# Performance work log

Measured on AMD Instinct MI355X. Metric: run time of the kernel, lower is better.

Reference implementation:

```python
import jax, jax.numpy as jnp
import numpy as np

MASK_VALUE = -1e10  # matches module's -10000000000.0


def setup_inputs() -> dict:
    key = jax.random.key(0)
    k1, k2, k3, k4, k5 = jax.random.split(key, 5)
    B, NQ, NKV, D = 32, 32, 8, 128
    NUM_PAGES, TPP, PAGES_PER_SLOT = 4096, 16, 128
    query = jax.random.normal(k1, (B, 1, NQ, D), dtype=jnp.float32)
    key_pages = jax.random.normal(k2, (NKV, NUM_PAGES, TPP, D), dtype=jnp.float32)
    value_pages = jax.random.normal(k3, (NKV, NUM_PAGES, TPP, D), dtype=jnp.float32)
    page_map = jax.random.randint(k4, (B, PAGES_PER_SLOT), 0, NUM_PAGES, dtype=jnp.int32)
    seq_lengths = jax.random.randint(k5, (B,), 1, PAGES_PER_SLOT * TPP + 1, dtype=jnp.int32)
    return {
        "query": query,
        "key_pages": key_pages,
        "value_pages": value_pages,
        "page_map": page_map,
        "seq_lengths": seq_lengths,
    }


def reference(query, key_pages, value_pages, page_map, seq_lengths):
    """Paged attention, decode mode (single query token per sequence, GQA).

    query:       [B, 1, NQ, D]
    key_pages:   [NKV, NUM_PAGES, TPP, D]
    value_pages: [NKV, NUM_PAGES, TPP, D]
    page_map:    [B, P] page indices per sequence
    seq_lengths: [B] valid kv tokens per sequence
    """
    B, _, NQ, D = query.shape
    NKV, _, TPP, _ = key_pages.shape
    G = NQ // NKV  # GQA group size
    # take last query position -> [B, NKV, G, D]
    q = query[:, -1].reshape(B, NKV, G, D)
    # gather pages per sequence: [NKV, B, P, TPP, D] -> [B, NKV, S, D]
    k = jnp.moveaxis(key_pages[:, page_map], 0, 1).reshape(B, NKV, -1, D)
    v = jnp.moveaxis(value_pages[:, page_map], 0, 1).reshape(B, NKV, -1, D)
    S = k.shape[2]
    scores = jnp.einsum("bkgd,bksd->bkgs", q, k)  # [B, NKV, G, S]
    valid = jnp.arange(S)[None, :] < seq_lengths[:, None]  # [B, S]
    scores = jnp.where(valid[:, None, None, :], scores, MASK_VALUE)
    weights = jax.nn.softmax(scores, axis=-1)
    out = jnp.einsum("bkgs,bksd->bkgd", weights, v)  # [B, NKV, G, D]
    return out.reshape(B, 1, NQ, D)
```

## Files before the change

kernel.cpp:

```cpp
#include <hip/hip_runtime.h>
#include <math.h>

#define NB      32
#define NKV     8
#define NQ      32
#define GQ      4
#define DH      128
#define TPP     16
#define PPS     128
#define NPAGES  4096
#define NSPLIT  8
#define PAGE_F  (TPP*DH)
#define PART_F  (GQ*DH + 2*GQ)

__global__ __launch_bounds__(256) void pa_partial(
    const float* __restrict__ query,
    const float* __restrict__ key_pages,
    const float* __restrict__ value_pages,
    const int*   __restrict__ page_map,
    const int*   __restrict__ seq_lengths,
    float*       __restrict__ ws)
{
    const int blk = blockIdx.x;
    const int sp  = blk & (NSPLIT - 1);
    const int kv  = (blk >> 3) & (NKV - 1);
    const int b   = blk >> 6;
    const int tid = threadIdx.x;

    const int seq     = seq_lengths[b];
    const int n_pages = (seq + TPP - 1) / TPP;
    if (sp >= n_pages) return;

    __shared__ __align__(16) float kbuf[TPP * DH];
    __shared__ __align__(16) float vbuf[TPP * DH];
    __shared__ float s_sc[GQ][TPP];

    const int lane = tid & 63;
    const int wv   = tid >> 6;
    const int tok  = wv * 4 + (lane >> 4);
    const int l16  = lane & 15;
    const int d0   = l16 * 8;

    const int d  = tid & 127;
    const int gA = tid >> 7;
    const int gB = gA + 2;

    float qreg[GQ][8];
    #pragma unroll
    for (int g = 0; g < GQ; ++g) {
        const float4* qp = (const float4*)(query + (size_t)((b * NQ + kv * GQ + g) * DH + d0));
        const float4 a = qp[0], c = qp[1];
        qreg[g][0] = a.x; qreg[g][1] = a.y; qreg[g][2] = a.z; qreg[g][3] = a.w;
        qreg[g][4] = c.x; qreg[g][5] = c.y; qreg[g][6] = c.z; qreg[g][7] = c.w;
    }

    float mA = -INFINITY, mB = -INFINITY;
    float lA = 0.f, lB = 0.f;
    float accA = 0.f, accB = 0.f;

    for (int p = sp; p < n_pages; p += NSPLIT) {
        const int pg = page_map[b * PPS + p];
        const float4* kg = (const float4*)(key_pages   + (size_t)(kv * NPAGES + pg) * PAGE_F);
        const float4* vg = (const float4*)(value_pages + (size_t)(kv * NPAGES + pg) * PAGE_F);

        __syncthreads();
        {
            float4* kb = (float4*)kbuf;
            float4* vb = (float4*)vbuf;
            kb[tid]       = kg[tid];
            kb[tid + 256] = kg[tid + 256];
            vb[tid]       = vg[tid];
            vb[tid + 256] = vg[tid + 256];
        }
        __syncthreads();

        float part0, part1, part2, part3;
        {
            const float4 k0 = *(const float4*)&kbuf[tok * DH + d0];
            const float4 k1 = *(const float4*)&kbuf[tok * DH + d0 + 4];
            part0 = qreg[0][0]*k0.x + qreg[0][1]*k0.y + qreg[0][2]*k0.z + qreg[0][3]*k0.w
                  + qreg[0][4]*k1.x + qreg[0][5]*k1.y + qreg[0][6]*k1.z + qreg[0][7]*k1.w;
            part1 = qreg[1][0]*k0.x + qreg[1][1]*k0.y + qreg[1][2]*k0.z + qreg[1][3]*k0.w
                  + qreg[1][4]*k1.x + qreg[1][5]*k1.y + qreg[1][6]*k1.z + qreg[1][7]*k1.w;
            part2 = qreg[2][0]*k0.x + qreg[2][1]*k0.y + qreg[2][2]*k0.z + qreg[2][3]*k0.w
                  + qreg[2][4]*k1.x + qreg[2][5]*k1.y + qreg[2][6]*k1.z + qreg[2][7]*k1.w;
            part3 = qreg[3][0]*k0.x + qreg[3][1]*k0.y + qreg[3][2]*k0.z + qreg[3][3]*k0.w
                  + qreg[3][4]*k1.x + qreg[3][5]*k1.y + qreg[3][6]*k1.z + qreg[3][7]*k1.w;
            #pragma unroll
            for (int off = 8; off >= 1; off >>= 1) {
                part0 += __shfl_xor(part0, off);
                part1 += __shfl_xor(part1, off);
                part2 += __shfl_xor(part2, off);
                part3 += __shfl_xor(part3, off);
            }
        }
        const int tglob = p * TPP + tok;
        if (l16 < GQ) {
            const float val = (l16 == 0) ? part0 : (l16 == 1) ? part1
                            : (l16 == 2) ? part2 : part3;
            s_sc[l16][tok] = (tglob < seq) ? val : -1e30f;
        }
        __syncthreads();

        float sA[TPP], sB[TPP];
        #pragma unroll
        for (int t = 0; t < TPP; ++t) { sA[t] = s_sc[gA][t]; sB[t] = s_sc[gB][t]; }

        float pA = -1e30f, pB = -1e30f;
        #pragma unroll
        for (int t = 0; t < TPP; ++t) { pA = fmaxf(pA, sA[t]); pB = fmaxf(pB, sB[t]); }

        const float mnA = fmaxf(mA, pA), mnB = fmaxf(mB, pB);
        const float scA = __expf(mA - mnA), scB = __expf(mB - mnB);
        mA = mnA; mB = mnB;

        float sumA = 0.f, sumB = 0.f;
        #pragma unroll
        for (int t = 0; t < TPP; ++t) {
            sA[t] = __expf(sA[t] - mnA); sumA += sA[t];
            sB[t] = __expf(sB[t] - mnB); sumB += sB[t];
        }
        lA = lA * scA + sumA;
        lB = lB * scB + sumB;
        accA *= scA;
        accB *= scB;

        #pragma unroll
        for (int t = 0; t < TPP; ++t) {
            const float v = vbuf[t * DH + d];
            accA += sA[t] * v;
            accB += sB[t] * v;
        }
    }

    float* base = ws + (size_t)blk * PART_F;
    base[gA * DH + d] = accA;
    base[gB * DH + d] = accB;
    if (d == 0) {
        base[GQ * DH + gA]      = mA;
        base[GQ * DH + GQ + gA] = lA;
        base[GQ * DH + gB]      = mB;
        base[GQ * DH + GQ + gB] = lB;
    }
}

__global__ __launch_bounds__(256) void pa_combine(
    const float* __restrict__ ws,
    const int*   __restrict__ seq_lengths,
    float*       __restrict__ out)
{
    const int blk = blockIdx.x;
    const int b   = blk >> 3;
    const int kv  = blk & 7;
    const int tid = threadIdx.x;
    const int d   = tid & 127;
    const int gA  = tid >> 7;
    const int gB  = gA + 2;

    const int seq     = seq_lengths[b];
    const int n_pages = (seq + TPP - 1) / TPP;
    const int ns      = (n_pages < NSPLIT) ? n_pages : NSPLIT;

    const float* base0 = ws + (size_t)blk * NSPLIT * PART_F;

    float MA = -INFINITY, MB = -INFINITY;
    for (int si = 0; si < ns; ++si) {
        const float* p = base0 + si * PART_F;
        MA = fmaxf(MA, p[GQ * DH + gA]);
        MB = fmaxf(MB, p[GQ * DH + gB]);
    }

    float LA = 0.f, LB = 0.f, oA = 0.f, oB = 0.f;
    for (int si = 0; si < ns; ++si) {
        const float* p = base0 + si * PART_F;
        const float eA = __expf(p[GQ * DH + gA] - MA);
        const float eB = __expf(p[GQ * DH + gB] - MB);
        LA += p[GQ * DH + GQ + gA] * eA;
        LB += p[GQ * DH + GQ + gB] * eB;
        oA += p[gA * DH + d] * eA;
        oB += p[gB * DH + d] * eB;
    }

    float* ob = out + (size_t)(b * NQ + kv * GQ) * DH;
    ob[gA * DH + d] = oA / LA;
    ob[gB * DH + d] = oB / LB;
}

extern "C" void kernel_launch(void* const* d_in, const int* in_sizes, int n_in,
                              void* d_out, int out_size, void* d_ws, size_t ws_size,
                              hipStream_t stream)
{
    const float* query       = (const float*)d_in[0];
    const float* key_pages   = (const float*)d_in[1];
    const float* value_pages = (const float*)d_in[2];
    const int*   page_map    = (const int*)d_in[3];
    const int*   seq_lengths = (const int*)d_in[4];
    float*       out         = (float*)d_out;
    float*       ws          = (float*)d_ws;

    pa_partial<<<NB * NKV * NSPLIT, 256, 0, stream>>>(
        query, key_pages, value_pages, page_map, seq_lengths, ws);
    pa_combine<<<NB * NKV, 256, 0, stream>>>(ws, seq_lengths, out);
}
```

Baseline: 61.24 us.

## Double-buffer KV pages in LDS using async global-to-LDS loads

```diff
diff --git a/kernel.cpp b/kernel.cpp
--- a/kernel.cpp
+++ b/kernel.cpp
@@ -1,5 +1,6 @@
 #include <hip/hip_runtime.h>
 #include <math.h>
+#include <stdint.h>
 
 #define NB      32
 #define NKV     8
@@ -12,6 +13,10 @@
 #define NSPLIT  8
 #define PAGE_F  (TPP*DH)
 #define PART_F  (GQ*DH + 2*GQ)
+
+#define GLOAD16(gsrc, ldst) \
+    __builtin_amdgcn_global_load_lds((const __attribute__((address_space(1))) uint32_t*)(gsrc), \
+                                     (__attribute__((address_space(3))) uint32_t*)(ldst), 16, 0, 0)
 
 __global__ __launch_bounds__(256) void pa_partial(
     const float* __restrict__ query,
@@ -31,8 +36,8 @@
     const int n_pages = (seq + TPP - 1) / TPP;
     if (sp >= n_pages) return;
 
-    __shared__ __align__(16) float kbuf[TPP * DH];
-    __shared__ __align__(16) float vbuf[TPP * DH];
+    __shared__ __align__(16) float kbuf[2][TPP * DH];
+    __shared__ __align__(16) float vbuf[2][TPP * DH];
     __shared__ float s_sc[GQ][TPP];
 
     const int lane = tid & 63;
@@ -54,30 +59,36 @@
         qreg[g][4] = c.x; qreg[g][5] = c.y; qreg[g][6] = c.z; qreg[g][7] = c.w;
     }
 
+    const float4* kbase = (const float4*)(key_pages   + (size_t)kv * NPAGES * PAGE_F);
+    const float4* vbase = (const float4*)(value_pages + (size_t)kv * NPAGES * PAGE_F);
+
+    auto stage = [&](int buf, int pg) {
+        const float4* kg = kbase + (size_t)pg * (PAGE_F / 4);
+        const float4* vg = vbase + (size_t)pg * (PAGE_F / 4);
+        GLOAD16(kg + wv * 128 +       lane, &kbuf[buf][wv * 512]);
+        GLOAD16(kg + wv * 128 +  64 + lane, &kbuf[buf][wv * 512 + 256]);
+        GLOAD16(vg + wv * 128 +       lane, &vbuf[buf][wv * 512]);
+        GLOAD16(vg + wv * 128 +  64 + lane, &vbuf[buf][wv * 512 + 256]);
+    };
+
     float mA = -INFINITY, mB = -INFINITY;
     float lA = 0.f, lB = 0.f;
     float accA = 0.f, accB = 0.f;
 
-    for (int p = sp; p < n_pages; p += NSPLIT) {
-        const int pg = page_map[b * PPS + p];
-        const float4* kg = (const float4*)(key_pages   + (size_t)(kv * NPAGES + pg) * PAGE_F);
-        const float4* vg = (const float4*)(value_pages + (size_t)(kv * NPAGES + pg) * PAGE_F);
-
-        __syncthreads();
-        {
-            float4* kb = (float4*)kbuf;
-            float4* vb = (float4*)vbuf;
-            kb[tid]       = kg[tid];
-            kb[tid + 256] = kg[tid + 256];
-            vb[tid]       = vg[tid];
-            vb[tid + 256] = vg[tid + 256];
-        }
-        __syncthreads();
+    stage(0, page_map[b * PPS + sp]);
+    asm volatile("s_waitcnt vmcnt(0)" ::: "memory");
+    __builtin_amdgcn_s_barrier();
+    asm volatile("" ::: "memory");
+
+    int cur = 0;
+    for (int p = sp; p < n_pages; p += NSPLIT, cur ^= 1) {
+        const int pn = p + NSPLIT;
+        if (pn < n_pages) stage(cur ^ 1, page_map[b * PPS + pn]);
 
         float part0, part1, part2, part3;
         {
-            const float4 k0 = *(const float4*)&kbuf[tok * DH + d0];
-            const float4 k1 = *(const float4*)&kbuf[tok * DH + d0 + 4];
+            const float4 k0 = *(const float4*)&kbuf[cur][tok * DH + d0];
+            const float4 k1 = *(const float4*)&kbuf[cur][tok * DH + d0 + 4];
             part0 = qreg[0][0]*k0.x + qreg[0][1]*k0.y + qreg[0][2]*k0.z + qreg[0][3]*k0.w
                   + qreg[0][4]*k1.x + qreg[0][5]*k1.y + qreg[0][6]*k1.z + qreg[0][7]*k1.w;
             part1 = qreg[1][0]*k0.x + qreg[1][1]*k0.y + qreg[1][2]*k0.z + qreg[1][3]*k0.w
@@ -100,7 +111,9 @@
                             : (l16 == 2) ? part2 : part3;
             s_sc[l16][tok] = (tglob < seq) ? val : -1e30f;
         }
-        __syncthreads();
+        asm volatile("s_waitcnt lgkmcnt(0)" ::: "memory");
+        __builtin_amdgcn_s_barrier();
+        asm volatile("" ::: "memory");
 
         float sA[TPP], sB[TPP];
         #pragma unroll
@@ -127,10 +140,12 @@
 
         #pragma unroll
         for (int t = 0; t < TPP; ++t) {
-            const float v = vbuf[t * DH + d];
+            const float v = vbuf[cur][t * DH + d];
             accA += sA[t] * v;
             accB += sB[t] * v;
         }
+
+        __syncthreads();
     }
 
     float* base = ws + (size_t)blk * PART_F;
```

Measured after the change: 62.48 us. +2.0%, slower.
